# Kernel tuning notes

Measured on AMD Instinct MI355X. Metric: run time of the kernel, lower is better.

## Reference

```python
import jax, jax.numpy as jnp
import numpy as np

NH = 12          # num attention heads
EPS = 1e-6       # layer-norm eps
B, T_, S_, H, E, IE = 8, 8, 196, 768, 4, 768  # IE = intermediate_size // num_experts


def layernorm(x, g, b):
    m = jnp.mean(x, axis=-1, keepdims=True)
    v = jnp.var(x, axis=-1, keepdims=True)
    return (x - m) / jnp.sqrt(v + EPS) * g + b


def mha(x, qkv_w, qkv_b, proj_w, proj_b):
    # x: [B', N, H]
    Bp, N, Hh = x.shape
    hd = Hh // NH
    qkv = (x @ qkv_w + qkv_b).reshape(Bp, N, 3, NH, hd).transpose(2, 0, 3, 1, 4)
    q, k, v = qkv[0], qkv[1], qkv[2]                      # [B', nh, N, hd]
    attn = jax.nn.softmax(jnp.einsum('bhqd,bhkd->bhqk', q, k) * (hd ** -0.5), axis=-1)
    out = jnp.einsum('bhqk,bhkd->bhqd', attn, v).transpose(0, 2, 1, 3).reshape(Bp, N, Hh)
    return out @ proj_w + proj_b


def moe_mlp(x, gate_up, down, eids):
    # x: [B, N, H]; gate_up: [E, H, 2*IE]; down: [E, IE, H]; eids: [N]
    sel = jax.nn.one_hot(eids, gate_up.shape[0], dtype=x.dtype)  # [N, E]
    gu = jnp.einsum('bnh,ehk,ne->bnk', x, gate_up, sel)          # per-token expert gate+up
    gate, up = gu[..., :IE], gu[..., IE:]
    inter = jax.nn.silu(gate) * up                               # SwiGLU
    return jnp.einsum('bni,eih,ne->bnh', inter, down, sel)


def setup_inputs() -> dict:
    key = jax.random.key(0)
    ks = jax.random.split(key, 16)
    w = lambda k, shp: (jax.random.normal(k, shp, dtype=jnp.float32) * 0.02)
    inp = {
        'x': jax.random.normal(ks[0], (B, T_ * S_, H), dtype=jnp.float32),
        'qkv_w_s': w(ks[1], (H, 3 * H)), 'qkv_b_s': jnp.zeros((3 * H,), jnp.float32),
        'proj_w_s': w(ks[2], (H, H)),    'proj_b_s': jnp.zeros((H,), jnp.float32),
        'qkv_w_t': w(ks[3], (H, 3 * H)), 'qkv_b_t': jnp.zeros((3 * H,), jnp.float32),
        'proj_w_t': w(ks[4], (H, H)),    'proj_b_t': jnp.zeros((H,), jnp.float32),
        'ln_s_g': jnp.ones((H,), jnp.float32), 'ln_s_b': jnp.zeros((H,), jnp.float32),
        'ln_t_g': jnp.ones((H,), jnp.float32), 'ln_t_b': jnp.zeros((H,), jnp.float32),
        'ln_m_g': jnp.ones((H,), jnp.float32), 'ln_m_b': jnp.zeros((H,), jnp.float32),
        'gate_up_proj': w(ks[5], (E, H, 2 * IE)),
        'down_proj': w(ks[6], (E, IE, H)),
        'T': T_, 'S': S_,
        'expert_ids': jax.random.randint(ks[7], (T_ * S_,), 0, E, dtype=jnp.int32),
    }
    return inp


def reference(x, qkv_w_s, qkv_b_s, proj_w_s, proj_b_s,
              qkv_w_t, qkv_b_t, proj_w_t, proj_b_t,
              ln_s_g, ln_s_b, ln_t_g, ln_t_b, ln_m_g, ln_m_b,
              gate_up_proj, down_proj, T, S, expert_ids):
    Bb, N, Hh = x.shape
    # 1) spatial attention over S patches within each of B*T frames
    xs = layernorm(x, ln_s_g, ln_s_b).reshape(Bb * T, S, Hh)
    xs = mha(xs, qkv_w_s, qkv_b_s, proj_w_s, proj_b_s).reshape(Bb, T * S, Hh)
    x = x + xs
    # 2) temporal attention over T frames at each of B*S spatial positions
    xt = layernorm(x, ln_t_g, ln_t_b).reshape(Bb, T, S, Hh).transpose(0, 2, 1, 3).reshape(Bb * S, T, Hh)
    xt = mha(xt, qkv_w_t, qkv_b_t, proj_w_t, proj_b_t)
    xt = xt.reshape(Bb, S, T, Hh).transpose(0, 2, 1, 3).reshape(Bb, T * S, Hh)
    x = x + xt
    # 3) token-routed MoE MLP
    x = x + moe_mlp(layernorm(x, ln_m_g, ln_m_b), gate_up_proj, down_proj, expert_ids)
    return x
```

## Files before the change

### kernel.cpp

```cpp
#include <hip/hip_runtime.h>

typedef __bf16 bf16;
typedef bf16 bf16x8 __attribute__((ext_vector_type(8)));
typedef float f32x4 __attribute__((ext_vector_type(4)));

#define BB 8
#define TT 8
#define SS 196
#define NTOK 1568
#define ROWS 12544
#define HH 768
#define HD 64

__device__ __forceinline__ void gload16(const void* g, void* l) {
  __builtin_amdgcn_global_load_lds(
      (const __attribute__((address_space(1))) void*)g,
      (__attribute__((address_space(3))) void*)l, 16, 0, 0);
}

#define BAR() do { asm volatile("" ::: "memory"); __builtin_amdgcn_s_barrier(); \
                   asm volatile("" ::: "memory"); } while (0)
#define VM2() asm volatile("s_waitcnt vmcnt(2)" ::: "memory")
#define VM0() asm volatile("s_waitcnt vmcnt(0)" ::: "memory")

__global__ __launch_bounds__(256)
void transpose_w(const float* __restrict__ in, bf16* __restrict__ out, int K, int N) {
  in  += (size_t)blockIdx.z * K * N;
  out += (size_t)blockIdx.z * K * N;
  __shared__ float tile[64][65];
  const int k0 = blockIdx.x * 64, n0 = blockIdx.y * 64;
  const int tx = threadIdx.x & 63, ty = threadIdx.x >> 6;
  #pragma unroll
  for (int rr = ty; rr < 64; rr += 4)
    tile[rr][tx] = in[(size_t)(k0 + rr) * N + n0 + tx];
  __syncthreads();
  #pragma unroll
  for (int rr = ty; rr < 64; rr += 4)
    out[(size_t)(n0 + rr) * K + k0 + tx] = (bf16)tile[tx][rr];
}

__global__ __launch_bounds__(256)
void ln_kernel(const float* __restrict__ x, const float* __restrict__ g,
               const float* __restrict__ b, bf16* __restrict__ out) {
  const int row = blockIdx.x * 4 + (threadIdx.x >> 6);
  const int lane = threadIdx.x & 63;
  const float* xr = x + (size_t)row * HH;
  float v[12];
  float sum = 0.f, sq = 0.f;
  #pragma unroll
  for (int i = 0; i < 12; ++i) {
    v[i] = xr[lane + i * 64];
    sum += v[i];
    sq += v[i] * v[i];
  }
  #pragma unroll
  for (int off = 32; off > 0; off >>= 1) {
    sum += __shfl_xor(sum, off);
    sq  += __shfl_xor(sq, off);
  }
  const float mean = sum * (1.f / 768.f);
  const float var = sq * (1.f / 768.f) - mean * mean;
  const float inv = rsqrtf(var + 1e-6f);
  bf16* op = out + (size_t)row * HH;
  #pragma unroll
  for (int i = 0; i < 12; ++i) {
    const int c = lane + i * 64;
    op[c] = (bf16)((v[i] - mean) * inv * g[c] + b[c]);
  }
}

template<bool MOE, bool BIAS, bool RESID, bool OBF16>
__global__ __launch_bounds__(512, 2)
void gemm8p(const bf16* __restrict__ A, const bf16* __restrict__ BT,
            const float* __restrict__ bias, const float* __restrict__ resid,
            float* __restrict__ outF, bf16* __restrict__ outB,
            int N, int K, int NMT,
            const int* __restrict__ perm, const int4* __restrict__ descs,
            const int* __restrict__ meta) {
  __shared__ __align__(16) bf16 lds[2 * 32768];
  __shared__ int rowLds[256];

  const int tid = threadIdx.x;
  int M0 = 0, N0, ncnt = 32;
  if constexpr (MOE) {
    if ((int)blockIdx.x >= meta[0]) return;
    int4 d = descs[blockIdx.x];
    BT += (size_t)d.x * N * K;
    ncnt = d.z;
    N0 = blockIdx.y * 256;
    if (tid < 256) {
      const int nl = tid >> 3, b = tid & 7;
      const int n = perm[d.y + (nl < ncnt ? nl : ncnt - 1)];
      rowLds[tid] = b * NTOK + n;
    }
    __syncthreads();
  } else {
    const int G = gridDim.x;
    const int q = G >> 3, r = G & 7, xcd = blockIdx.x & 7, pos = blockIdx.x >> 3;
    const int work = (xcd < r ? xcd * (q + 1) : r * (q + 1) + (xcd - r) * q) + pos;
    const int mt = work % NMT, nt = work / NMT;
    M0 = mt * 256;
    N0 = nt * 256;
  }

  const int w = tid >> 6, lane = tid & 63;
  const int wr = w >> 2, wc = w & 3;
  const int lr = lane & 15, lg = lane >> 4;

  const int srow0 = tid >> 3;
  const int srow1 = 64 + srow0;
  const int sseg0 = (tid & 7) ^ (srow0 & 7);
  const int sseg1 = (tid & 7) ^ (srow1 & 7);
  int ar00, ar01, ar10, ar11;
  if constexpr (MOE) {
    ar00 = rowLds[srow0];        ar01 = rowLds[srow1];
    ar10 = rowLds[128 + srow0];  ar11 = rowLds[128 + srow1];
  } else {
    ar00 = M0 + srow0;           ar01 = M0 + srow1;
    ar10 = M0 + 128 + srow0;     ar11 = M0 + 128 + srow1;
  }
  const bf16* aP00 = A + (size_t)ar00 * K + sseg0 * 8;
  const bf16* aP01 = A + (size_t)ar01 * K + sseg1 * 8;
  const bf16* aP10 = A + (size_t)ar10 * K + sseg0 * 8;
  const bf16* aP11 = A + (size_t)ar11 * K + sseg1 * 8;
  const bf16* bP00 = BT + (size_t)(N0 + srow0) * K + sseg0 * 8;
  const bf16* bP01 = BT + (size_t)(N0 + srow1) * K + sseg1 * 8;
  const bf16* bP10 = BT + (size_t)(N0 + 128 + srow0) * K + sseg0 * 8;
  const bf16* bP11 = BT + (size_t)(N0 + 128 + srow1) * K + sseg1 * 8;

  auto STG = [&](const bf16* P0, const bf16* P1, int dstoff, int kt) {
    bf16* d_ = lds + dstoff;
    gload16(P0 + (size_t)kt * 64, d_ + tid * 8);
    gload16(P1 + (size_t)kt * 64, d_ + 4096 + tid * 8);
  };
  auto LDA = [&](int dd, int mh, bf16x8* D) {
    #pragma unroll
    for (int mf = 0; mf < 4; ++mf) {
      const int ra = wr * 128 + mh * 64 + mf * 16 + lr;
      const bf16* p = lds + dd * 32768 + ra * 64;
      D[mf * 2 + 0] = *(const bf16x8*)(p + ((lg ^ (lr & 7)) * 8));
      D[mf * 2 + 1] = *(const bf16x8*)(p + (((4 + lg) ^ (lr & 7)) * 8));
    }
  };
  auto LDB = [&](int dd, int nh, bf16x8* D) {
    #pragma unroll
    for (int nf = 0; nf < 2; ++nf) {
      const int rb = wc * 64 + nh * 32 + nf * 16 + lr;
      const bf16* p = lds + dd * 32768 + 16384 + rb * 64;
      D[nf * 2 + 0] = *(const bf16x8*)(p + ((lg ^ (lr & 7)) * 8));
      D[nf * 2 + 1] = *(const bf16x8*)(p + (((4 + lg) ^ (lr & 7)) * 8));
    }
  };

  f32x4 acc[8][4] = {};
  auto MM = [&](const bf16x8* AF, const bf16x8* BF, int mh, int nh) {
    __builtin_amdgcn_s_setprio(1);
    #pragma unroll
    for (int mf = 0; mf < 4; ++mf)
      #pragma unroll
      for (int nf = 0; nf < 2; ++nf) {
        f32x4 c = acc[mh * 4 + mf][nh * 2 + nf];
        c = __builtin_amdgcn_mfma_f32_16x16x32_bf16(AF[mf * 2 + 0], BF[nf * 2 + 0], c, 0, 0, 0);
        c = __builtin_amdgcn_mfma_f32_16x16x32_bf16(AF[mf * 2 + 1], BF[nf * 2 + 1], c, 0, 0, 0);
        acc[mh * 4 + mf][nh * 2 + nf] = c;
      }
    __builtin_amdgcn_s_setprio(0);
  };

  const int NI = K >> 7;

  STG(aP00, aP01, 0, 0);
  STG(aP10, aP11, 8192, 0);
  STG(bP00, bP01, 16384, 0);
  STG(bP10, bP11, 24576, 0);
  STG(aP00, aP01, 32768, 1);
  VM2();
  BAR();

  bf16x8 a[8], b[4], b2[4];
  for (int i = 0; i < NI; ++i) {
    const bool last = (i == NI - 1);
    const int k1 = 2 * i + 1, k2 = 2 * i + 2, k3 = 2 * i + 3;
    STG(aP10, aP11, 32768 + 8192, k1);
    LDA(0, 0, a); LDB(0, 0, b);
    MM(a, b, 0, 0);
    BAR();
    STG(bP00, bP01, 32768 + 16384, k1);
    LDB(0, 1, b2);
    MM(a, b2, 0, 1);
    BAR();
    STG(bP10, bP11, 32768 + 24576, k1);
    LDA(0, 1, a);
    MM(a, b2, 1, 1);
    BAR();
    if (!last) STG(aP00, aP01, 0, k2);
    LDB(0, 0, b);
    MM(a, b, 1, 0);
    if (!last) { VM2(); } else { VM0(); }
    BAR();
    if (!last) STG(aP10, aP11, 8192, k2);
    LDA(1, 0, a); LDB(1, 0, b);
    MM(a, b, 0, 0);
    BAR();
    if (!last) STG(bP00, bP01, 16384, k2);
    LDB(1, 1, b2);
    MM(a, b2, 0, 1);
    BAR();
    if (!last) STG(bP10, bP11, 24576, k2);
    LDA(1, 1, a);
    MM(a, b2, 1, 1);
    BAR();
    if (!last) STG(aP00, aP01, 32768, k3);
    LDB(1, 0, b);
    MM(a, b, 1, 0);
    if (!last) { VM2(); BAR(); }
  }

  #pragma unroll
  for (int m = 0; m < 8; ++m) {
    #pragma unroll
    for (int j = 0; j < 4; ++j) {
      const int r = wr * 128 + m * 16 + lg * 4 + j;
      if (MOE && ((r >> 3) >= ncnt)) continue;
      const size_t grow = MOE ? (size_t)rowLds[r] : (size_t)(M0 + r);
      const size_t rbase = grow * N;
      #pragma unroll
      for (int n = 0; n < 4; ++n) {
        const int gcol = N0 + wc * 64 + n * 16 + lr;
        float v = acc[m][n][j];
        if constexpr (BIAS)  v += bias[gcol];
        if constexpr (RESID) v += resid[rbase + gcol];
        if constexpr (OBF16) outB[rbase + gcol] = (bf16)v;
        else                 outF[rbase + gcol] = v;
      }
    }
  }
}

template<bool MOE, bool BIAS, bool RESID, bool OBF16>
__global__ __launch_bounds__(256, 2)
void gemmU(const bf16* __restrict__ A, const bf16* __restrict__ BT,
           const float* __restrict__ bias, const float* __restrict__ resid,
           float* __restrict__ outF, bf16* __restrict__ outB,
           int N, int K, int G, int NTN,
           const int* __restrict__ perm, const int4* __restrict__ descs,
           const int* __restrict__ meta) {
  __shared__ __align__(16) bf16 lds[3 * 8192];

  const int tid = threadIdx.x;
  int M0, N0;
  {
    const int id = blockIdx.x;
    const int q = G >> 3, r = G & 7, xcd = id & 7, pos = id >> 3;
    const int work = (xcd < r ? xcd * (q + 1) : r * (q + 1) + (xcd - r) * q) + pos;
    const int mt = work / NTN, nt = work - mt * NTN;
    M0 = mt * 128;
    N0 = nt * 128;
  }

  const int w = tid >> 6, lane = tid & 63;
  const int wr = w >> 1, wc = w & 1;

  size_t aG[2], bG[2]; int aL[2], bL[2];
  #pragma unroll
  for (int i = 0; i < 2; ++i) {
    const int c = tid + i * 256;
    const int row = c >> 2, seg = (c & 3) ^ ((c >> 3) & 3);
    aG[i] = (size_t)(M0 + row) * K + seg * 8;
    aL[i] = c * 8;
    bG[i] = (size_t)(N0 + row) * K + seg * 8;
    bL[i] = 4096 + c * 8;
  }

#define STGU(tt) { bf16* bp = lds + ((tt) % 3) * 8192; const int ko = (tt) << 5; \
    gload16(A + aG[0] + ko, bp + aL[0]);                                        \
    gload16(A + aG[1] + ko, bp + aL[1]);                                        \
    gload16(BT + bG[0] + ko, bp + bL[0]);                                       \
    gload16(BT + bG[1] + ko, bp + bL[1]); }

  STGU(0);
  STGU(1);

  f32x4 acc[4][4] = {};
  const int lr = lane & 15, lg = lane >> 4;
  const int xr = ((lr >> 1) & 3) * 8;
  const int NT = K >> 5;

  for (int t = 0; t < NT; ++t) {
    if (t + 1 < NT) { asm volatile("s_waitcnt vmcnt(4)" ::: "memory"); }
    else            { asm volatile("s_waitcnt vmcnt(0)" ::: "memory"); }
    __builtin_amdgcn_s_barrier();
    asm volatile("" ::: "memory");

    const bf16* Ab = lds + (t % 3) * 8192;
    const bf16* Bb = Ab + 4096;
    bf16x8 af[4], bf_[4];
    #pragma unroll
    for (int m = 0; m < 4; ++m)
      af[m] = *(const bf16x8*)&Ab[(wr * 64 + m * 16 + lr) * 32 + ((lg * 8) ^ xr)];
    #pragma unroll
    for (int n = 0; n < 4; ++n)
      bf_[n] = *(const bf16x8*)&Bb[(wc * 64 + n * 16 + lr) * 32 + ((lg * 8) ^ xr)];

    __builtin_amdgcn_s_setprio(1);
    #pragma unroll
    for (int m = 0; m < 4; ++m)
      #pragma unroll
      for (int n = 0; n < 4; ++n)
        acc[m][n] = __builtin_amdgcn_mfma_f32_16x16x32_bf16(af[m], bf_[n], acc[m][n], 0, 0, 0);
    __builtin_amdgcn_s_setprio(0);

    asm volatile("" ::: "memory");
    __builtin_amdgcn_s_barrier();
    asm volatile("" ::: "memory");
    if (t + 2 < NT) STGU(t + 2);
  }
#undef STGU

  #pragma unroll
  for (int m = 0; m < 4; ++m) {
    #pragma unroll
    for (int j = 0; j < 4; ++j) {
      const int r = wr * 64 + m * 16 + lg * 4 + j;
      const size_t rbase = (size_t)(M0 + r) * N;
      #pragma unroll
      for (int n = 0; n < 4; ++n) {
        const int gcol = N0 + wc * 64 + n * 16 + lr;
        float v = acc[m][n][j];
        if constexpr (BIAS)  v += bias[gcol];
        if constexpr (RESID) v += resid[rbase + gcol];
        if constexpr (OBF16) outB[rbase + gcol] = (bf16)v;
        else                 outF[rbase + gcol] = v;
      }
    }
  }
}

#define SPAD 208
#define VST 232
__global__ __launch_bounds__(512)
void attn_spatial(const bf16* __restrict__ qkv, bf16* __restrict__ out) {
  __shared__ __align__(16) bf16 Ks[SPAD * 64];
  __shared__ __align__(16) bf16 Vt[64 * VST];
  __shared__ __align__(16) bf16 Pb[8][16 * VST];

  const int bp = blockIdx.x, h = blockIdx.y;
  const int tid = threadIdx.x;
  const int w = tid >> 6, lane = tid & 63;
  const int lr = lane & 15, lg = lane >> 4;
  const size_t base = (size_t)bp * SS * 2304 + h * HD;

  for (int cb = w * 64; cb < SPAD * 8; cb += 512) {
    const int c = cb + lane;
    const int row = c >> 3, seg = c & 7;
    const int srow = row < SS ? row : SS - 1;
    const int sseg = seg ^ (row & 7);
    gload16(qkv + base + (size_t)srow * 2304 + 768 + sseg * 8, Ks + cb * 8);
  }
  for (int t = tid; t < 224 * 8; t += 512) {
    const int k = t >> 3, dseg = t & 7;
    const int sk = k < SS ? k : SS - 1;
    bf16x8 v = *(const bf16x8*)(qkv + base + (size_t)sk * 2304 + 1536 + dseg * 8);
    #pragma unroll
    for (int i = 0; i < 8; ++i) Vt[(dseg * 8 + i) * VST + k] = v[i];
  }
  bf16* Pw = Pb[w];
  for (int i = lane; i < 256; i += 64)
    Pw[(i >> 4) * VST + 208 + (i & 15)] = (bf16)0.f;
  __syncthreads();

  for (int t = w; t < 13; t += 8) {
    const int q0 = t * 16;
    const int qr = q0 + lr;
    const bf16* qp = qkv + base + (size_t)(qr < SS ? qr : SS - 1) * 2304 + lg * 8;
    const bf16x8 af0 = *(const bf16x8*)qp;
    const bf16x8 af1 = *(const bf16x8*)(qp + 32);

    f32x4 sc[13];
    #pragma unroll
    for (int f = 0; f < 13; ++f) sc[f] = (f32x4){0.f, 0.f, 0.f, 0.f};
    #pragma unroll
    for (int f = 0; f < 13; ++f) {
      const int key = f * 16 + lr;
      const bf16x8 bv0 = *(const bf16x8*)&Ks[key * 64 + ((lg) ^ (key & 7)) * 8];
      const bf16x8 bv1 = *(const bf16x8*)&Ks[key * 64 + ((4 + lg) ^ (key & 7)) * 8];
      sc[f] = __builtin_amdgcn_mfma_f32_16x16x32_bf16(af0, bv0, sc[f], 0, 0, 0);
      sc[f] = __builtin_amdgcn_mfma_f32_16x16x32_bf16(af1, bv1, sc[f], 0, 0, 0);
    }
    #pragma unroll
    for (int f = 0; f < 13; ++f)
      #pragma unroll
      for (int j = 0; j < 4; ++j) sc[f][j] *= 0.125f;
    if (192 + lr >= SS)
      #pragma unroll
      for (int j = 0; j < 4; ++j) sc[12][j] = -1e30f;

    float mx[4], ls[4];
    #pragma unroll
    for (int j = 0; j < 4; ++j) {
      float m = sc[0][j];
      #pragma unroll
      for (int f = 1; f < 13; ++f) m = fmaxf(m, sc[f][j]);
      #pragma unroll
      for (int off = 1; off < 16; off <<= 1) m = fmaxf(m, __shfl_xor(m, off));
      mx[j] = m;
    }
    #pragma unroll
    for (int j = 0; j < 4; ++j) ls[j] = 0.f;
    #pragma unroll
    for (int f = 0; f < 13; ++f) {
      #pragma unroll
      for (int j = 0; j < 4; ++j) {
        const float p = __expf(sc[f][j] - mx[j]);
        ls[j] += p;
        Pw[(lg * 4 + j) * VST + f * 16 + lr] = (bf16)p;
      }
    }
    #pragma unroll
    for (int j = 0; j < 4; ++j) {
      #pragma unroll
      for (int off = 1; off < 16; off <<= 1) ls[j] += __shfl_xor(ls[j], off);
      ls[j] = 1.f / ls[j];
    }

    f32x4 oacc[4];
    #pragma unroll
    for (int n = 0; n < 4; ++n) oacc[n] = (f32x4){0.f, 0.f, 0.f, 0.f};
    #pragma unroll
    for (int kb = 0; kb < 7; ++kb) {
      const bf16x8 pa = *(const bf16x8*)&Pw[lr * VST + kb * 32 + lg * 8];
      #pragma unroll
      for (int n = 0; n < 4; ++n) {
        const bf16x8 bv = *(const bf16x8*)&Vt[(n * 16 + lr) * VST + kb * 32 + lg * 8];
        oacc[n] = __builtin_amdgcn_mfma_f32_16x16x32_bf16(pa, bv, oacc[n], 0, 0, 0);
      }
    }
    #pragma unroll
    for (int j = 0; j < 4; ++j) {
      const int row = q0 + lg * 4 + j;
      if (row < SS) {
        bf16* op = out + ((size_t)bp * SS + row) * 768 + h * HD;
        #pragma unroll
        for (int n = 0; n < 4; ++n) op[n * 16 + lr] = (bf16)(oacc[n][j] * ls[j]);
      }
    }
  }
}

__global__ __launch_bounds__(256)
void attn_temporal(const bf16* __restrict__ qkv, bf16* __restrict__ out) {
  const int pair = blockIdx.x * 4 + (threadIdx.x >> 6);
  const int lane = threadIdx.x & 63;
  const int h = pair % 12;
  const int bs = pair / 12;
  const int b = bs / SS, s = bs - b * SS;
  const size_t row0 = (size_t)b * NTOK + s;
  const int q = lane >> 3, k = lane & 7;
  const bf16* qr = qkv + (row0 + (size_t)q * SS) * 2304 + h * HD;
  const bf16* kr = qkv + (row0 + (size_t)k * SS) * 2304 + 768 + h * HD;
  float sc = 0.f;
  #pragma unroll
  for (int j = 0; j < 8; ++j) {
    bf16x8 qv = ((const bf16x8*)qr)[j];
    bf16x8 kv = ((const bf16x8*)kr)[j];
    #pragma unroll
    for (int d = 0; d < 8; ++d) sc += (float)qv[d] * (float)kv[d];
  }
  sc *= 0.125f;
  float mxv = sc;
  #pragma unroll
  for (int off = 1; off < 8; off <<= 1) mxv = fmaxf(mxv, __shfl_xor(mxv, off));
  float p = __expf(sc - mxv);
  float sum = p;
  #pragma unroll
  for (int off = 1; off < 8; off <<= 1) sum += __shfl_xor(sum, off);
  p /= sum;

  const int dg = lane & 7;
  float o[8] = {0, 0, 0, 0, 0, 0, 0, 0};
  #pragma unroll
  for (int kk = 0; kk < 8; ++kk) {
    const float pk = __shfl(p, (lane & 56) + kk);
    const bf16* vr = qkv + (row0 + (size_t)kk * SS) * 2304 + 1536 + h * HD + dg * 8;
    bf16x8 vv = *(const bf16x8*)vr;
    #pragma unroll
    for (int j = 0; j < 8; ++j) o[j] += pk * (float)vv[j];
  }
  bf16* op = out + (row0 + (size_t)q * SS) * 768 + h * HD + dg * 8;
  bf16x8 ov;
  #pragma unroll
  for (int j = 0; j < 8; ++j) ov[j] = (bf16)o[j];
  *(bf16x8*)op = ov;
}

__global__ __launch_bounds__(256)
void sort_moe(const int* __restrict__ eids, int* __restrict__ perm,
              int4* __restrict__ descs, int* __restrict__ meta) {
  __shared__ int cnt[4], base[4], cur[4];
  const int tid = threadIdx.x;
  if (tid < 4) cnt[tid] = 0;
  __syncthreads();
  for (int n = tid; n < NTOK; n += 256) atomicAdd(&cnt[eids[n]], 1);
  __syncthreads();
  if (tid == 0) {
    int off = 0;
    for (int e = 0; e < 4; ++e) { base[e] = off; cur[e] = off; off += cnt[e]; }
  }
  __syncthreads();
  for (int n = tid; n < NTOK; n += 256) {
    const int pos = atomicAdd(&cur[eids[n]], 1);
    perm[pos] = n;
  }
  if (tid == 0) {
    int t = 0;
    for (int e = 0; e < 4; ++e)
      for (int st = 0; st < cnt[e]; st += 32) {
        const int c = cnt[e] - st;
        descs[t++] = make_int4(e, base[e] + st, c < 32 ? c : 32, 0);
      }
    meta[0] = t;
  }
}

__global__ __launch_bounds__(256)
void silu_mul(const bf16* __restrict__ gu, bf16* __restrict__ out) {
  const size_t i = ((size_t)blockIdx.x * 256 + threadIdx.x) * 4;
  if (i >= (size_t)ROWS * 768) return;
  const size_t row = i / 768, c = i - row * 768;
  const bf16* g = gu + row * 1536 + c;
  const bf16* u = gu + row * 1536 + 768 + c;
  bf16* o = out + i;
  #pragma unroll
  for (int j = 0; j < 4; ++j) {
    const float gv = (float)g[j], uv = (float)u[j];
    const float sv = gv / (1.f + __expf(-gv));
    o[j] = (bf16)(sv * uv);
  }
}

extern "C" void kernel_launch(void* const* d_in, const int* in_sizes, int n_in,
                              void* d_out, int out_size, void* d_ws, size_t ws_size,
                              hipStream_t stream) {
  (void)in_sizes; (void)n_in; (void)out_size; (void)ws_size;
  const float* x        = (const float*)d_in[0];
  const float* qkv_w_s  = (const float*)d_in[1];
  const float* qkv_b_s  = (const float*)d_in[2];
  const float* proj_w_s = (const float*)d_in[3];
  const float* proj_b_s = (const float*)d_in[4];
  const float* qkv_w_t  = (const float*)d_in[5];
  const float* qkv_b_t  = (const float*)d_in[6];
  const float* proj_w_t = (const float*)d_in[7];
  const float* proj_b_t = (const float*)d_in[8];
  const float* ln_s_g   = (const float*)d_in[9];
  const float* ln_s_b   = (const float*)d_in[10];
  const float* ln_t_g   = (const float*)d_in[11];
  const float* ln_t_b   = (const float*)d_in[12];
  const float* ln_m_g   = (const float*)d_in[13];
  const float* ln_m_b   = (const float*)d_in[14];
  const float* gate_up  = (const float*)d_in[15];
  const float* down_w   = (const float*)d_in[16];
  const int* expert_ids = (const int*)d_in[19];
  float* out = (float*)d_out;

  char* ws = (char*)d_ws;
  bf16* qkvsT   = (bf16*)(ws + 0);
  bf16* projsT  = (bf16*)(ws + 3538944);
  bf16* qkvtT   = (bf16*)(ws + 4718592);
  bf16* projtT  = (bf16*)(ws + 8257536);
  bf16* guT     = (bf16*)(ws + 9437184);
  bf16* downT   = (bf16*)(ws + 18874368);
  bf16* lnbuf   = (bf16*)(ws + 23592960);
  bf16* qkvbuf  = (bf16*)(ws + 42860544);
  bf16* attnbuf = (bf16*)(ws + 100663296);
  float* x1     = (float*)(ws + 119930880);
  int*  perm    = (int*)(ws + 158466048);
  int4* descs   = (int4*)(ws + 158472320);
  int*  meta    = (int*)(ws + 158473952);

  const dim3 blk(256);
  const dim3 blk512(512);

  transpose_w<<<dim3(12, 36, 1), blk, 0, stream>>>(qkv_w_s, qkvsT, 768, 2304);
  transpose_w<<<dim3(12, 12, 1), blk, 0, stream>>>(proj_w_s, projsT, 768, 768);
  transpose_w<<<dim3(12, 36, 1), blk, 0, stream>>>(qkv_w_t, qkvtT, 768, 2304);
  transpose_w<<<dim3(12, 12, 1), blk, 0, stream>>>(proj_w_t, projtT, 768, 768);
  transpose_w<<<dim3(12, 24, 4), blk, 0, stream>>>(gate_up, guT, 768, 1536);
  transpose_w<<<dim3(12, 12, 4), blk, 0, stream>>>(down_w, downT, 768, 768);

  ln_kernel<<<3136, blk, 0, stream>>>(x, ln_s_g, ln_s_b, lnbuf);
  gemm8p<false, true, false, true><<<dim3(49 * 9), blk512, 0, stream>>>(
      lnbuf, qkvsT, qkv_b_s, nullptr, nullptr, qkvbuf, 2304, 768, 49,
      nullptr, nullptr, nullptr);
  attn_spatial<<<dim3(64, 12), blk512, 0, stream>>>(qkvbuf, attnbuf);
  gemmU<false, true, true, false><<<dim3(98 * 6), blk, 0, stream>>>(
      attnbuf, projsT, proj_b_s, x, x1, nullptr, 768, 768, 98 * 6, 6,
      nullptr, nullptr, nullptr);

  ln_kernel<<<3136, blk, 0, stream>>>(x1, ln_t_g, ln_t_b, lnbuf);
  gemm8p<false, true, false, true><<<dim3(49 * 9), blk512, 0, stream>>>(
      lnbuf, qkvtT, qkv_b_t, nullptr, nullptr, qkvbuf, 2304, 768, 49,
      nullptr, nullptr, nullptr);
  attn_temporal<<<4704, blk, 0, stream>>>(qkvbuf, attnbuf);
  gemmU<false, true, true, false><<<dim3(98 * 6), blk, 0, stream>>>(
      attnbuf, projtT, proj_b_t, x1, out, nullptr, 768, 768, 98 * 6, 6,
      nullptr, nullptr, nullptr);

  ln_kernel<<<3136, blk, 0, stream>>>(out, ln_m_g, ln_m_b, lnbuf);
  sort_moe<<<1, blk, 0, stream>>>(expert_ids, perm, descs, meta);
  gemm8p<true, false, false, true><<<dim3(56, 6), blk512, 0, stream>>>(
      lnbuf, guT, nullptr, nullptr, nullptr, qkvbuf, 1536, 768, 0,
      perm, descs, meta);
  silu_mul<<<9408, blk, 0, stream>>>(qkvbuf, lnbuf);
  gemm8p<true, false, true, false><<<dim3(56, 3), blk512, 0, stream>>>(
      lnbuf, downT, nullptr, out, out, nullptr, 768, 768, 0,
      perm, descs, meta);
}
```

Baseline: 410.9 us.

## Fuse SwiGLU into gate-up GEMM epilogue and restructure gemm8p pipeline

The gate_up weights are transposed with gate and up columns interleaved in 32-column groups, so each 256-wide N tile holds matching gate and up columns. The MoE gate-up GEMM then applies silu(g)*u in its epilogue and writes a 768-wide bf16 intermediate, which removes the separate silu_mul kernel and the round trip of the 1536-wide buffer. The gemm8p main loop is also rescheduled, with B prefetched first, lgkmcnt waits and sched barriers around each MFMA block, and vmcnt(4), and launch bounds drop to one block per SM. This may reduce occupancy, and the unused MOE template path is removed from gemmU.

```diff
diff --git a/kernel.cpp b/kernel.cpp
--- a/kernel.cpp
+++ b/kernel.cpp
@@ -18,10 +18,14 @@
       (__attribute__((address_space(3))) void*)l, 16, 0, 0);
 }
 
-#define BAR() do { asm volatile("" ::: "memory"); __builtin_amdgcn_s_barrier(); \
-                   asm volatile("" ::: "memory"); } while (0)
-#define VM2() asm volatile("s_waitcnt vmcnt(2)" ::: "memory")
-#define VM0() asm volatile("s_waitcnt vmcnt(0)" ::: "memory")
+#define VMC4() asm volatile("s_waitcnt vmcnt(4)" ::: "memory")
+#define VMC0() asm volatile("s_waitcnt vmcnt(0)" ::: "memory")
+#define PRE_MFMA() do { asm volatile("" ::: "memory");                      \
+    __builtin_amdgcn_s_barrier();                                           \
+    asm volatile("s_waitcnt lgkmcnt(0)" ::: "memory");                      \
+    __builtin_amdgcn_sched_barrier(0); } while (0)
+#define POST_MFMA() do { asm volatile("" ::: "memory");                     \
+    __builtin_amdgcn_s_barrier(); asm volatile("" ::: "memory"); } while (0)
 
 __global__ __launch_bounds__(256)
 void transpose_w(const float* __restrict__ in, bf16* __restrict__ out, int K, int N) {
@@ -33,6 +37,26 @@
   #pragma unroll
   for (int rr = ty; rr < 64; rr += 4)
     tile[rr][tx] = in[(size_t)(k0 + rr) * N + n0 + tx];
+  __syncthreads();
+  #pragma unroll
+  for (int rr = ty; rr < 64; rr += 4)
+    out[(size_t)(n0 + rr) * K + k0 + tx] = (bf16)tile[tx][rr];
+}
+
+__global__ __launch_bounds__(256)
+void transpose_gu(const float* __restrict__ in, bf16* __restrict__ out) {
+  const int K = 768, N = 1536;
+  in  += (size_t)blockIdx.z * K * N;
+  out += (size_t)blockIdx.z * K * N;
+  __shared__ float tile[64][65];
+  const int k0 = blockIdx.x * 64, n0 = blockIdx.y * 64;
+  const int tx = threadIdx.x & 63, ty = threadIdx.x >> 6;
+  const int s = n0 >> 6;
+  #pragma unroll
+  for (int rr = ty; rr < 64; rr += 4) {
+    const int src = (tx < 32) ? (s * 32 + tx) : (768 + s * 32 + tx - 32);
+    tile[rr][tx] = in[(size_t)(k0 + rr) * N + src];
+  }
   __syncthreads();
   #pragma unroll
   for (int rr = ty; rr < 64; rr += 4)
@@ -69,8 +93,8 @@
   }
 }
 
-template<bool MOE, bool BIAS, bool RESID, bool OBF16>
-__global__ __launch_bounds__(512, 2)
+template<bool MOE, bool BIAS, bool RESID, bool OBF16, bool GUFUSE>
+__global__ __launch_bounds__(512, 1)
 void gemm8p(const bf16* __restrict__ A, const bf16* __restrict__ BT,
             const float* __restrict__ bias, const float* __restrict__ resid,
             float* __restrict__ outF, bf16* __restrict__ outB,
@@ -110,7 +134,6 @@
   const int srow0 = tid >> 3;
   const int srow1 = 64 + srow0;
   const int sseg0 = (tid & 7) ^ (srow0 & 7);
-  const int sseg1 = (tid & 7) ^ (srow1 & 7);
   int ar00, ar01, ar10, ar11;
   if constexpr (MOE) {
     ar00 = rowLds[srow0];        ar01 = rowLds[srow1];
@@ -120,32 +143,31 @@
     ar10 = M0 + 128 + srow0;     ar11 = M0 + 128 + srow1;
   }
   const bf16* aP00 = A + (size_t)ar00 * K + sseg0 * 8;
-  const bf16* aP01 = A + (size_t)ar01 * K + sseg1 * 8;
+  const bf16* aP01 = A + (size_t)ar01 * K + sseg0 * 8;
   const bf16* aP10 = A + (size_t)ar10 * K + sseg0 * 8;
-  const bf16* aP11 = A + (size_t)ar11 * K + sseg1 * 8;
+  const bf16* aP11 = A + (size_t)ar11 * K + sseg0 * 8;
   const bf16* bP00 = BT + (size_t)(N0 + srow0) * K + sseg0 * 8;
-  const bf16* bP01 = BT + (size_t)(N0 + srow1) * K + sseg1 * 8;
+  const bf16* bP01 = BT + (size_t)(N0 + srow1) * K + sseg0 * 8;
   const bf16* bP10 = BT + (size_t)(N0 + 128 + srow0) * K + sseg0 * 8;
-  const bf16* bP11 = BT + (size_t)(N0 + 128 + srow1) * K + sseg1 * 8;
+  const bf16* bP11 = BT + (size_t)(N0 + 128 + srow1) * K + sseg0 * 8;
 
   auto STG = [&](const bf16* P0, const bf16* P1, int dstoff, int kt) {
-    bf16* d_ = lds + dstoff;
-    gload16(P0 + (size_t)kt * 64, d_ + tid * 8);
-    gload16(P1 + (size_t)kt * 64, d_ + 4096 + tid * 8);
+    gload16(P0 + (size_t)kt * 64, lds + dstoff + tid * 8);
+    gload16(P1 + (size_t)kt * 64, lds + dstoff + 4096 + tid * 8);
   };
-  auto LDA = [&](int dd, int mh, bf16x8* D) {
+  auto LDA = [&](int dd, int qm, bf16x8* D) {
     #pragma unroll
     for (int mf = 0; mf < 4; ++mf) {
-      const int ra = wr * 128 + mh * 64 + mf * 16 + lr;
+      const int ra = wr * 128 + qm * 64 + mf * 16 + lr;
       const bf16* p = lds + dd * 32768 + ra * 64;
       D[mf * 2 + 0] = *(const bf16x8*)(p + ((lg ^ (lr & 7)) * 8));
       D[mf * 2 + 1] = *(const bf16x8*)(p + (((4 + lg) ^ (lr & 7)) * 8));
     }
   };
-  auto LDB = [&](int dd, int nh, bf16x8* D) {
+  auto LDB = [&](int dd, int qn, bf16x8* D) {
     #pragma unroll
     for (int nf = 0; nf < 2; ++nf) {
-      const int rb = wc * 64 + nh * 32 + nf * 16 + lr;
+      const int rb = wc * 64 + qn * 32 + nf * 16 + lr;
       const bf16* p = lds + dd * 32768 + 16384 + rb * 64;
       D[nf * 2 + 0] = *(const bf16x8*)(p + ((lg ^ (lr & 7)) * 8));
       D[nf * 2 + 1] = *(const bf16x8*)(p + (((4 + lg) ^ (lr & 7)) * 8));
@@ -153,16 +175,16 @@
   };
 
   f32x4 acc[8][4] = {};
-  auto MM = [&](const bf16x8* AF, const bf16x8* BF, int mh, int nh) {
+  auto MM = [&](const bf16x8* AF, const bf16x8* BF, int qm, int qn) {
     __builtin_amdgcn_s_setprio(1);
     #pragma unroll
     for (int mf = 0; mf < 4; ++mf)
       #pragma unroll
       for (int nf = 0; nf < 2; ++nf) {
-        f32x4 c = acc[mh * 4 + mf][nh * 2 + nf];
+        f32x4 c = acc[qm * 4 + mf][qn * 2 + nf];
         c = __builtin_amdgcn_mfma_f32_16x16x32_bf16(AF[mf * 2 + 0], BF[nf * 2 + 0], c, 0, 0, 0);
         c = __builtin_amdgcn_mfma_f32_16x16x32_bf16(AF[mf * 2 + 1], BF[nf * 2 + 1], c, 0, 0, 0);
-        acc[mh * 4 + mf][nh * 2 + nf] = c;
+        acc[qm * 4 + mf][qn * 2 + nf] = c;
       }
     __builtin_amdgcn_s_setprio(0);
   };
@@ -173,47 +195,41 @@
   STG(aP10, aP11, 8192, 0);
   STG(bP00, bP01, 16384, 0);
   STG(bP10, bP11, 24576, 0);
-  STG(aP00, aP01, 32768, 1);
-  VM2();
-  BAR();
-
-  bf16x8 a[8], b[4], b2[4];
+  STG(bP00, bP01, 32768 + 16384, 1);
+  STG(bP10, bP11, 32768 + 24576, 1);
+  VMC4();
+  asm volatile("" ::: "memory");
+  __builtin_amdgcn_s_barrier();
+  asm volatile("" ::: "memory");
+
+  bf16x8 a[8], b0[4], b1[4];
   for (int i = 0; i < NI; ++i) {
-    const bool last = (i == NI - 1);
+    const bool more = (i + 1 < NI);
     const int k1 = 2 * i + 1, k2 = 2 * i + 2, k3 = 2 * i + 3;
+    LDA(0, 0, a); LDB(0, 0, b0);
+    STG(aP00, aP01, 32768, k1);
+    PRE_MFMA(); MM(a, b0, 0, 0); POST_MFMA();
+    LDB(0, 1, b1);
     STG(aP10, aP11, 32768 + 8192, k1);
-    LDA(0, 0, a); LDB(0, 0, b);
-    MM(a, b, 0, 0);
-    BAR();
-    STG(bP00, bP01, 32768 + 16384, k1);
-    LDB(0, 1, b2);
-    MM(a, b2, 0, 1);
-    BAR();
-    STG(bP10, bP11, 32768 + 24576, k1);
+    PRE_MFMA(); MM(a, b1, 0, 1); POST_MFMA();
     LDA(0, 1, a);
-    MM(a, b2, 1, 1);
-    BAR();
-    if (!last) STG(aP00, aP01, 0, k2);
-    LDB(0, 0, b);
-    MM(a, b, 1, 0);
-    if (!last) { VM2(); } else { VM0(); }
-    BAR();
-    if (!last) STG(aP10, aP11, 8192, k2);
-    LDA(1, 0, a); LDB(1, 0, b);
-    MM(a, b, 0, 0);
-    BAR();
-    if (!last) STG(bP00, bP01, 16384, k2);
-    LDB(1, 1, b2);
-    MM(a, b2, 0, 1);
-    BAR();
-    if (!last) STG(bP10, bP11, 24576, k2);
+    if (more) STG(bP00, bP01, 16384, k2);
+    PRE_MFMA(); MM(a, b1, 1, 1); POST_MFMA();
+    if (more) STG(bP10, bP11, 24576, k2);
+    if (more) { VMC4(); } else { VMC0(); }
+    PRE_MFMA(); MM(a, b0, 1, 0); POST_MFMA();
+    LDA(1, 0, a); LDB(1, 0, b0);
+    if (more) STG(aP00, aP01, 0, k2);
+    PRE_MFMA(); MM(a, b0, 0, 0); POST_MFMA();
+    LDB(1, 1, b1);
+    if (more) STG(aP10, aP11, 8192, k2);
+    PRE_MFMA(); MM(a, b1, 0, 1); POST_MFMA();
     LDA(1, 1, a);
-    MM(a, b2, 1, 1);
-    BAR();
-    if (!last) STG(aP00, aP01, 32768, k3);
-    LDB(1, 0, b);
-    MM(a, b, 1, 0);
-    if (!last) { VM2(); BAR(); }
+    if (more) STG(bP00, bP01, 32768 + 16384, k3);
+    PRE_MFMA(); MM(a, b1, 1, 1); POST_MFMA();
+    if (more) STG(bP10, bP11, 32768 + 24576, k3);
+    if (more) { VMC4(); }
+    PRE_MFMA(); MM(a, b0, 1, 0); POST_MFMA();
   }
 
   #pragma unroll
@@ -223,28 +239,36 @@
       const int r = wr * 128 + m * 16 + lg * 4 + j;
       if (MOE && ((r >> 3) >= ncnt)) continue;
       const size_t grow = MOE ? (size_t)rowLds[r] : (size_t)(M0 + r);
-      const size_t rbase = grow * N;
-      #pragma unroll
-      for (int n = 0; n < 4; ++n) {
-        const int gcol = N0 + wc * 64 + n * 16 + lr;
-        float v = acc[m][n][j];
-        if constexpr (BIAS)  v += bias[gcol];
-        if constexpr (RESID) v += resid[rbase + gcol];
-        if constexpr (OBF16) outB[rbase + gcol] = (bf16)v;
-        else                 outF[rbase + gcol] = v;
+      if constexpr (GUFUSE) {
+        const size_t rbase = grow * 768;
+        #pragma unroll
+        for (int n = 0; n < 2; ++n) {
+          const int icol = (N0 >> 1) + wc * 32 + n * 16 + lr;
+          const float g = acc[m][n][j], u = acc[m][n + 2][j];
+          outB[rbase + icol] = (bf16)(g / (1.f + __expf(-g)) * u);
+        }
+      } else {
+        const size_t rbase = grow * N;
+        #pragma unroll
+        for (int n = 0; n < 4; ++n) {
+          const int gcol = N0 + wc * 64 + n * 16 + lr;
+          float v = acc[m][n][j];
+          if constexpr (BIAS)  v += bias[gcol];
+          if constexpr (RESID) v += resid[rbase + gcol];
+          if constexpr (OBF16) outB[rbase + gcol] = (bf16)v;
+          else                 outF[rbase + gcol] = v;
+        }
       }
     }
   }
 }
 
-template<bool MOE, bool BIAS, bool RESID, bool OBF16>
+template<bool BIAS, bool RESID, bool OBF16>
 __global__ __launch_bounds__(256, 2)
 void gemmU(const bf16* __restrict__ A, const bf16* __restrict__ BT,
            const float* __restrict__ bias, const float* __restrict__ resid,
            float* __restrict__ outF, bf16* __restrict__ outB,
-           int N, int K, int G, int NTN,
-           const int* __restrict__ perm, const int4* __restrict__ descs,
-           const int* __restrict__ meta) {
+           int N, int K, int G, int NTN) {
   __shared__ __align__(16) bf16 lds[3 * 8192];
 
   const int tid = threadIdx.x;
@@ -519,22 +543,6 @@
         descs[t++] = make_int4(e, base[e] + st, c < 32 ? c : 32, 0);
       }
     meta[0] = t;
-  }
-}
-
-__global__ __launch_bounds__(256)
-void silu_mul(const bf16* __restrict__ gu, bf16* __restrict__ out) {
-  const size_t i = ((size_t)blockIdx.x * 256 + threadIdx.x) * 4;
-  if (i >= (size_t)ROWS * 768) return;
-  const size_t row = i / 768, c = i - row * 768;
-  const bf16* g = gu + row * 1536 + c;
-  const bf16* u = gu + row * 1536 + 768 + c;
-  bf16* o = out + i;
-  #pragma unroll
-  for (int j = 0; j < 4; ++j) {
-    const float gv = (float)g[j], uv = (float)u[j];
-    const float sv = gv / (1.f + __expf(-gv));
-    o[j] = (bf16)(sv * uv);
   }
 }
 
@@ -584,34 +592,31 @@
   transpose_w<<<dim3(12, 12, 1), blk, 0, stream>>>(proj_w_s, projsT, 768, 768);
   transpose_w<<<dim3(12, 36, 1), blk, 0, stream>>>(qkv_w_t, qkvtT, 768, 2304);
   transpose_w<<<dim3(12, 12, 1), blk, 0, stream>>>(proj_w_t, projtT, 768, 768);
-  transpose_w<<<dim3(12, 24, 4), blk, 0, stream>>>(gate_up, guT, 768, 1536);
+  transpose_gu<<<dim3(12, 24, 4), blk, 0, stream>>>(gate_up, guT);
   transpose_w<<<dim3(12, 12, 4), blk, 0, stream>>>(down_w, downT, 768, 768);
 
   ln_kernel<<<3136, blk, 0, stream>>>(x, ln_s_g, ln_s_b, lnbuf);
-  gemm8p<false, true, false, true><<<dim3(49 * 9), blk512, 0, stream>>>(
+  gemm8p<false, true, false, true, false><<<dim3(49 * 9), blk512, 0, stream>>>(
       lnbuf, qkvsT, qkv_b_s, nullptr, nullptr, qkvbuf, 2304, 768, 49,
       nullptr, nullptr, nullptr);
   attn_spatial<<<dim3(64, 12), blk512, 0, stream>>>(qkvbuf, attnbuf);
-  gemmU<false, true, true, false><<<dim3(98 * 6), blk, 0, stream>>>(
-      attnbuf, projsT, proj_b_s, x, x1, nullptr, 768, 768, 98 * 6, 6,
-      nullptr, nullptr, nullptr);
+  gemmU<true, true, false><<<dim3(98 * 6), blk, 0, stream>>>(
+      attnbuf, projsT, proj_b_s, x, x1, nullptr, 768, 768, 98 * 6, 6);
 
   ln_kernel<<<3136, blk, 0, stream>>>(x1, ln_t_g, ln_t_b, lnbuf);
-  gemm8p<false, true, false, true><<<dim3(49 * 9), blk512, 0, stream>>>(
+  gemm8p<false, true, false, true, false><<<dim3(49 * 9), blk512, 0, stream>>>(
       lnbuf, qkvtT, qkv_b_t, nullptr, nullptr, qkvbuf, 2304, 768, 49,
       nullptr, nullptr, nullptr);
   attn_temporal<<<4704, blk, 0, stream>>>(qkvbuf, attnbuf);
-  gemmU<false, true, true, false><<<dim3(98 * 6), blk, 0, stream>>>(
-      attnbuf, projtT, proj_b_t, x1, out, nullptr, 768, 768, 98 * 6, 6,
-      nullptr, nullptr, nullptr);
+  gemmU<true, true, false><<<dim3(98 * 6), blk, 0, stream>>>(
+      attnbuf, projtT, proj_b_t, x1, out, nullptr, 768, 768, 98 * 6, 6);
 
   ln_kernel<<<3136, blk, 0, stream>>>(out, ln_m_g, ln_m_b, lnbuf);
   sort_moe<<<1, blk, 0, stream>>>(expert_ids, perm, descs, meta);
-  gemm8p<true, false, false, true><<<dim3(56, 6), blk512, 0, stream>>>(
+  gemm8p<true, false, false, true, true><<<dim3(56, 6), blk512, 0, stream>>>(
       lnbuf, guT, nullptr, nullptr, nullptr, qkvbuf, 1536, 768, 0,
       perm, descs, meta);
-  silu_mul<<<9408, blk, 0, stream>>>(qkvbuf, lnbuf);
-  gemm8p<true, false, true, false><<<dim3(56, 3), blk512, 0, stream>>>(
-      lnbuf, downT, nullptr, out, out, nullptr, 768, 768, 0,
+  gemm8p<true, false, true, false, false><<<dim3(56, 3), blk512, 0, stream>>>(
+      qkvbuf, downT, nullptr, out, out, nullptr, 768, 768, 0,
       perm, descs, meta);
 }
```

Result: no change. 409.8 us (-0.3%).
